# Kernel optimization log

Hardware: AMD Instinct MI355X
Metric: run time of the kernel (lower is better)

Reference implementation:

```python
import jax, jax.numpy as jnp
import numpy as np

EPS = 1e-6

def _complex_log(x):
    # real = log(clamp_min(|x|, eps)); imag = pi where x < 0 else 0
    real = jnp.log(jnp.maximum(jnp.abs(x), EPS))
    imag = jnp.where(x < 0, np.float32(np.pi), np.float32(0.0))
    return jax.lax.complex(real, imag)

def _clogaddexp(a, b):
    # stable log(exp(a)+exp(b)) for complex a, b (shift by max of real parts)
    m = jnp.maximum(a.real, b.real)
    return jnp.log(jnp.exp(a - m) + jnp.exp(b - m)) + m

def _min_gru(h, g):
    # log-space minGRU linear recurrence over the last axis
    log_coeffs = -jax.nn.softplus(g)                      # [..., L] real
    log_values = _complex_log(h) - jax.nn.softplus(-g)    # [..., L] complex
    a_star = jnp.cumsum(log_coeffs, axis=-1)              # [..., L] real
    z = log_values - a_star                               # complex
    log_h0_plus_b_star = jax.lax.associative_scan(_clogaddexp, z, axis=-1)
    log_h = a_star + log_h0_plus_b_star
    return jnp.exp(log_h).real

def _min_gru_bidirectional(x):
    # x: [B, H, L] with H divisible by 4
    H = x.shape[1]
    fore, back = x[:, : H // 2], x[:, H // 2 :]
    fh, fg = fore[:, : H // 4], fore[:, H // 4 :]
    back = jnp.flip(back, axis=2)  # matches torch .flip(2) for [B,H,L]
    bh, bg = back[:, : H // 4], back[:, H // 4 :]
    out_f = _min_gru(fh, fg)
    out_b = jnp.flip(_min_gru(bh, bg), axis=2)
    return jnp.concatenate([out_f, out_b], axis=1)  # [B, H/2, L]

def setup_inputs() -> dict:
    key = jax.random.key(0)
    x = jax.random.normal(key, (16, 512, 4096), dtype=jnp.float32)
    return {"x": x}

def reference(x):
    return _min_gru_bidirectional(x)
```

## Files before the change

kernel.cpp:

```cpp
#include <hip/hip_runtime.h>


#define T_LEN 4096
#define CHUNK 16
#define NTHR 256

__global__ __launch_bounds__(NTHR) void mingru_bidir_kernel(
    const float* __restrict__ x, float* __restrict__ out) {
  const int row = blockIdx.x;
  const int b   = row >> 8;
  const int c   = row & 255;
  const int tid = threadIdx.x;
  const int lane = tid & 63;
  const int wid  = tid >> 6;
  const bool bwd = (c >= 128);
  const int j = c & 127;

  const float* __restrict__ hptr =
      x + ((size_t)b * 512 + (bwd ? 256 : 0) + j) * T_LEN;
  const float* __restrict__ gptr =
      x + ((size_t)b * 512 + (bwd ? 384 : 128) + j) * T_LEN;
  float* __restrict__ optr = out + ((size_t)b * 256 + c) * T_LEN;

  const int t0 = bwd ? (T_LEN - CHUNK - (tid << 4)) : (tid << 4);

  float cc[CHUNK], vv[CHUNK];

  #pragma unroll
  for (int q = 0; q < 4; ++q) {
    const float4 h4 = *reinterpret_cast<const float4*>(hptr + t0 + 4 * q);
    const float4 g4 = *reinterpret_cast<const float4*>(gptr + t0 + 4 * q);
    const float hs[4] = {h4.x, h4.y, h4.z, h4.w};
    const float gs[4] = {g4.x, g4.y, g4.z, g4.w};
    #pragma unroll
    for (int r = 0; r < 4; ++r) {
      const int e = 4 * q + r;
      const float h = hs[r];
      const float g = gs[r];
      const float ah = fmaxf(fabsf(h), 1e-6f);
      const float hp = (h < 0.0f) ? -ah : ah;
      const float eg  = __expf(-fabsf(g));
      const float inv = __builtin_amdgcn_rcpf(1.0f + eg);
      const float sg  = (g >= 0.0f) ? inv : eg * inv;
      cc[e] = 1.0f - sg;
      vv[e] = sg * hp;
    }
  }

  if (bwd) {
    #pragma unroll
    for (int e = 0; e < CHUNK / 2; ++e) {
      float t1 = cc[e]; cc[e] = cc[CHUNK - 1 - e]; cc[CHUNK - 1 - e] = t1;
      float t2 = vv[e]; vv[e] = vv[CHUNK - 1 - e]; vv[CHUNK - 1 - e] = t2;
    }
  }

  float C = cc[0], V = vv[0];
  #pragma unroll
  for (int e = 1; e < CHUNK; ++e) {
    V = cc[e] * V + vv[e];
    C = C * cc[e];
  }

  #pragma unroll
  for (int off = 1; off < 64; off <<= 1) {
    const float pc = __shfl_up(C, off);
    const float pv = __shfl_up(V, off);
    if (lane >= off) {
      V = C * pv + V;
      C = C * pc;
    }
  }

  __shared__ float sC[4], sV[4];
  if (lane == 63) { sC[wid] = C; sV[wid] = V; }
  __syncthreads();
  float acc = 0.0f;
  for (int w = 0; w < wid; ++w) acc = sC[w] * acc + sV[w];

  const float pC = __shfl_up(C, 1);
  const float pV = __shfl_up(V, 1);
  const float incoming = (lane == 0) ? acc : pC * acc + pV;

  float st = incoming;
  #pragma unroll
  for (int e = 0; e < CHUNK; ++e) {
    st = cc[e] * st + vv[e];
    vv[e] = st;
  }

  if (bwd) {
    #pragma unroll
    for (int e = 0; e < CHUNK / 2; ++e) {
      float t2 = vv[e]; vv[e] = vv[CHUNK - 1 - e]; vv[CHUNK - 1 - e] = t2;
    }
  }

  #pragma unroll
  for (int q = 0; q < 4; ++q) {
    *reinterpret_cast<float4*>(optr + t0 + 4 * q) =
        make_float4(vv[4 * q], vv[4 * q + 1], vv[4 * q + 2], vv[4 * q + 3]);
  }
}

extern "C" void kernel_launch(void* const* d_in, const int* in_sizes, int n_in,
                              void* d_out, int out_size, void* d_ws, size_t ws_size,
                              hipStream_t stream) {
  const float* x = (const float*)d_in[0];
  float* out = (float*)d_out;
  const int rows = 16 * 256;
  mingru_bidir_kernel<<<rows, NTHR, 0, stream>>>(x, out);
}
```

Baseline: 39.27 us.

## Interleave per-thread chunks for coalesced loads and run four independent scans

Each thread now loads four float4 pieces spaced 1024 elements apart instead of 16 contiguous elements, so a wavefront reads contiguous memory on each access. The row is therefore split into four independent 1024-long segments, each scanned across the block with its own wave shuffle scan and cross-wave combine, and the segments are chained serially. Backward rows use shfl_down scans instead of reversed register order. Launch bounds now request higher occupancy. The cost is four times as many shuffle-scan steps and more shared-memory combine work.

```diff
diff --git a/kernel.cpp b/kernel.cpp
--- a/kernel.cpp
+++ b/kernel.cpp
@@ -2,10 +2,9 @@
 
 
 #define T_LEN 4096
-#define CHUNK 16
 #define NTHR 256
 
-__global__ __launch_bounds__(NTHR) void mingru_bidir_kernel(
+__global__ __launch_bounds__(NTHR, 6) void mingru_bidir_kernel(
     const float* __restrict__ x, float* __restrict__ out) {
   const int row = blockIdx.x;
   const int b   = row >> 8;
@@ -22,19 +21,17 @@
       x + ((size_t)b * 512 + (bwd ? 384 : 128) + j) * T_LEN;
   float* __restrict__ optr = out + ((size_t)b * 256 + c) * T_LEN;
 
-  const int t0 = bwd ? (T_LEN - CHUNK - (tid << 4)) : (tid << 4);
-
-  float cc[CHUNK], vv[CHUNK];
+  float cc[4][4], vv[4][4];
 
   #pragma unroll
   for (int q = 0; q < 4; ++q) {
-    const float4 h4 = *reinterpret_cast<const float4*>(hptr + t0 + 4 * q);
-    const float4 g4 = *reinterpret_cast<const float4*>(gptr + t0 + 4 * q);
+    const int m0 = (q << 10) + (tid << 2);
+    const float4 h4 = *reinterpret_cast<const float4*>(hptr + m0);
+    const float4 g4 = *reinterpret_cast<const float4*>(gptr + m0);
     const float hs[4] = {h4.x, h4.y, h4.z, h4.w};
     const float gs[4] = {g4.x, g4.y, g4.z, g4.w};
     #pragma unroll
     for (int r = 0; r < 4; ++r) {
-      const int e = 4 * q + r;
       const float h = hs[r];
       const float g = gs[r];
       const float ah = fmaxf(fabsf(h), 1e-6f);
@@ -42,64 +39,103 @@
       const float eg  = __expf(-fabsf(g));
       const float inv = __builtin_amdgcn_rcpf(1.0f + eg);
       const float sg  = (g >= 0.0f) ? inv : eg * inv;
-      cc[e] = 1.0f - sg;
-      vv[e] = sg * hp;
+      const float co  = 1.0f - sg;
+      const float va  = sg * hp;
+      if (bwd) { cc[q][3 - r] = co; vv[q][3 - r] = va; }
+      else     { cc[q][r]     = co; vv[q][r]     = va; }
     }
   }
 
   if (bwd) {
     #pragma unroll
-    for (int e = 0; e < CHUNK / 2; ++e) {
-      float t1 = cc[e]; cc[e] = cc[CHUNK - 1 - e]; cc[CHUNK - 1 - e] = t1;
-      float t2 = vv[e]; vv[e] = vv[CHUNK - 1 - e]; vv[CHUNK - 1 - e] = t2;
+    for (int e = 0; e < 4; ++e) {
+      float t;
+      t = cc[0][e]; cc[0][e] = cc[3][e]; cc[3][e] = t;
+      t = cc[1][e]; cc[1][e] = cc[2][e]; cc[2][e] = t;
+      t = vv[0][e]; vv[0][e] = vv[3][e]; vv[3][e] = t;
+      t = vv[1][e]; vv[1][e] = vv[2][e]; vv[2][e] = t;
     }
   }
 
-  float C = cc[0], V = vv[0];
+  float C[4], V[4];
   #pragma unroll
-  for (int e = 1; e < CHUNK; ++e) {
-    V = cc[e] * V + vv[e];
-    C = C * cc[e];
-  }
-
-  #pragma unroll
-  for (int off = 1; off < 64; off <<= 1) {
-    const float pc = __shfl_up(C, off);
-    const float pv = __shfl_up(V, off);
-    if (lane >= off) {
-      V = C * pv + V;
-      C = C * pc;
+  for (int q = 0; q < 4; ++q) {
+    C[q] = cc[q][0]; V[q] = vv[q][0];
+    #pragma unroll
+    for (int e = 1; e < 4; ++e) {
+      V[q] = cc[q][e] * V[q] + vv[q][e];
+      C[q] = C[q] * cc[q][e];
     }
   }
 
-  __shared__ float sC[4], sV[4];
-  if (lane == 63) { sC[wid] = C; sV[wid] = V; }
-  __syncthreads();
-  float acc = 0.0f;
-  for (int w = 0; w < wid; ++w) acc = sC[w] * acc + sV[w];
-
-  const float pC = __shfl_up(C, 1);
-  const float pV = __shfl_up(V, 1);
-  const float incoming = (lane == 0) ? acc : pC * acc + pV;
-
-  float st = incoming;
-  #pragma unroll
-  for (int e = 0; e < CHUNK; ++e) {
-    st = cc[e] * st + vv[e];
-    vv[e] = st;
+  if (!bwd) {
+    #pragma unroll
+    for (int q = 0; q < 4; ++q) {
+      #pragma unroll
+      for (int off = 1; off < 64; off <<= 1) {
+        const float pc = __shfl_up(C[q], off);
+        const float pv = __shfl_up(V[q], off);
+        if (lane >= off) { V[q] = C[q] * pv + V[q]; C[q] = C[q] * pc; }
+      }
+    }
+  } else {
+    #pragma unroll
+    for (int q = 0; q < 4; ++q) {
+      #pragma unroll
+      for (int off = 1; off < 64; off <<= 1) {
+        const float pc = __shfl_down(C[q], off);
+        const float pv = __shfl_down(V[q], off);
+        if (lane < 64 - off) { V[q] = C[q] * pv + V[q]; C[q] = C[q] * pc; }
+      }
+    }
   }
 
-  if (bwd) {
+  __shared__ float sC[4][4], sV[4][4];
+  if (lane == (bwd ? 0 : 63)) {
     #pragma unroll
-    for (int e = 0; e < CHUNK / 2; ++e) {
-      float t2 = vv[e]; vv[e] = vv[CHUNK - 1 - e]; vv[CHUNK - 1 - e] = t2;
+    for (int q = 0; q < 4; ++q) { sC[wid][q] = C[q]; sV[wid][q] = V[q]; }
+  }
+  __syncthreads();
+
+  float myin[4];
+  float s = 0.0f;
+  if (!bwd) {
+    #pragma unroll
+    for (int q = 0; q < 4; ++q) {
+      #pragma unroll
+      for (int w = 0; w < 4; ++w) {
+        if (w == wid) myin[q] = s;
+        s = sC[w][q] * s + sV[w][q];
+      }
+    }
+  } else {
+    #pragma unroll
+    for (int q = 0; q < 4; ++q) {
+      #pragma unroll
+      for (int w = 3; w >= 0; --w) {
+        if (w == wid) myin[q] = s;
+        s = sC[w][q] * s + sV[w][q];
+      }
     }
   }
 
   #pragma unroll
   for (int q = 0; q < 4; ++q) {
-    *reinterpret_cast<float4*>(optr + t0 + 4 * q) =
-        make_float4(vv[4 * q], vv[4 * q + 1], vv[4 * q + 2], vv[4 * q + 3]);
+    const float pc = bwd ? __shfl_down(C[q], 1) : __shfl_up(C[q], 1);
+    const float pv = bwd ? __shfl_down(V[q], 1) : __shfl_up(V[q], 1);
+    const bool first = bwd ? (lane == 63) : (lane == 0);
+    float st = first ? myin[q] : pc * myin[q] + pv;
+
+    float o[4];
+    #pragma unroll
+    for (int e = 0; e < 4; ++e) {
+      st = cc[q][e] * st + vv[q][e];
+      o[e] = st;
+    }
+    const int qmem = bwd ? 3 - q : q;
+    const float4 o4 = bwd ? make_float4(o[3], o[2], o[1], o[0])
+                          : make_float4(o[0], o[1], o[2], o[3]);
+    *reinterpret_cast<float4*>(optr + (qmem << 10) + (tid << 2)) = o4;
   }
 }
 
```

After: 36.47 us. 1.08x faster.

## Use 1024 threads per row with 4 elements each and direction-aware scan

Applied to the files above, without the earlier changes.

Each row is now processed by 1024 threads, each owning a single float4 instead of 16 elements. The backward direction runs its wave and cross-wave scans in reverse order (shfl_down, descending wave loop) instead of flipping register arrays. The aim is coalesced contiguous loads per wave and more memory parallelism. The cost is a 16-wave block with a longer serial cross-wave combine and more scan work relative to the loads.

```diff
diff --git a/kernel.cpp b/kernel.cpp
--- a/kernel.cpp
+++ b/kernel.cpp
@@ -2,8 +2,7 @@
 
 
 #define T_LEN 4096
-#define CHUNK 16
-#define NTHR 256
+#define NTHR 1024
 
 __global__ __launch_bounds__(NTHR) void mingru_bidir_kernel(
     const float* __restrict__ x, float* __restrict__ out) {
@@ -22,85 +21,86 @@
       x + ((size_t)b * 512 + (bwd ? 384 : 128) + j) * T_LEN;
   float* __restrict__ optr = out + ((size_t)b * 256 + c) * T_LEN;
 
-  const int t0 = bwd ? (T_LEN - CHUNK - (tid << 4)) : (tid << 4);
+  const int m0 = tid << 2;
 
-  float cc[CHUNK], vv[CHUNK];
+  const float4 h4 = *reinterpret_cast<const float4*>(hptr + m0);
+  const float4 g4 = *reinterpret_cast<const float4*>(gptr + m0);
+  const float hs[4] = {h4.x, h4.y, h4.z, h4.w};
+  const float gs[4] = {g4.x, g4.y, g4.z, g4.w};
 
+  float cc[4], vv[4];
   #pragma unroll
-  for (int q = 0; q < 4; ++q) {
-    const float4 h4 = *reinterpret_cast<const float4*>(hptr + t0 + 4 * q);
-    const float4 g4 = *reinterpret_cast<const float4*>(gptr + t0 + 4 * q);
-    const float hs[4] = {h4.x, h4.y, h4.z, h4.w};
-    const float gs[4] = {g4.x, g4.y, g4.z, g4.w};
-    #pragma unroll
-    for (int r = 0; r < 4; ++r) {
-      const int e = 4 * q + r;
-      const float h = hs[r];
-      const float g = gs[r];
-      const float ah = fmaxf(fabsf(h), 1e-6f);
-      const float hp = (h < 0.0f) ? -ah : ah;
-      const float eg  = __expf(-fabsf(g));
-      const float inv = __builtin_amdgcn_rcpf(1.0f + eg);
-      const float sg  = (g >= 0.0f) ? inv : eg * inv;
-      cc[e] = 1.0f - sg;
-      vv[e] = sg * hp;
-    }
-  }
-
-  if (bwd) {
-    #pragma unroll
-    for (int e = 0; e < CHUNK / 2; ++e) {
-      float t1 = cc[e]; cc[e] = cc[CHUNK - 1 - e]; cc[CHUNK - 1 - e] = t1;
-      float t2 = vv[e]; vv[e] = vv[CHUNK - 1 - e]; vv[CHUNK - 1 - e] = t2;
-    }
+  for (int r = 0; r < 4; ++r) {
+    const float h = hs[r];
+    const float g = gs[r];
+    const float ah = fmaxf(fabsf(h), 1e-6f);
+    const float hp = (h < 0.0f) ? -ah : ah;
+    const float eg  = __expf(-fabsf(g));
+    const float inv = __builtin_amdgcn_rcpf(1.0f + eg);
+    const float sg  = (g >= 0.0f) ? inv : eg * inv;
+    const float co  = 1.0f - sg;
+    const float va  = sg * hp;
+    if (bwd) { cc[3 - r] = co; vv[3 - r] = va; }
+    else     { cc[r]     = co; vv[r]     = va; }
   }
 
   float C = cc[0], V = vv[0];
   #pragma unroll
-  for (int e = 1; e < CHUNK; ++e) {
+  for (int e = 1; e < 4; ++e) {
     V = cc[e] * V + vv[e];
     C = C * cc[e];
   }
 
-  #pragma unroll
-  for (int off = 1; off < 64; off <<= 1) {
-    const float pc = __shfl_up(C, off);
-    const float pv = __shfl_up(V, off);
-    if (lane >= off) {
-      V = C * pv + V;
-      C = C * pc;
+  if (!bwd) {
+    #pragma unroll
+    for (int off = 1; off < 64; off <<= 1) {
+      const float pc = __shfl_up(C, off);
+      const float pv = __shfl_up(V, off);
+      if (lane >= off) { V = C * pv + V; C = C * pc; }
+    }
+  } else {
+    #pragma unroll
+    for (int off = 1; off < 64; off <<= 1) {
+      const float pc = __shfl_down(C, off);
+      const float pv = __shfl_down(V, off);
+      if (lane < 64 - off) { V = C * pv + V; C = C * pc; }
     }
   }
 
-  __shared__ float sC[4], sV[4];
-  if (lane == 63) { sC[wid] = C; sV[wid] = V; }
+  __shared__ float sC[16], sV[16];
+  if (lane == (bwd ? 0 : 63)) { sC[wid] = C; sV[wid] = V; }
   __syncthreads();
-  float acc = 0.0f;
-  for (int w = 0; w < wid; ++w) acc = sC[w] * acc + sV[w];
 
-  const float pC = __shfl_up(C, 1);
-  const float pV = __shfl_up(V, 1);
-  const float incoming = (lane == 0) ? acc : pC * acc + pV;
-
-  float st = incoming;
-  #pragma unroll
-  for (int e = 0; e < CHUNK; ++e) {
-    st = cc[e] * st + vv[e];
-    vv[e] = st;
-  }
-
-  if (bwd) {
+  float myin = 0.0f;
+  float s = 0.0f;
+  if (!bwd) {
     #pragma unroll
-    for (int e = 0; e < CHUNK / 2; ++e) {
-      float t2 = vv[e]; vv[e] = vv[CHUNK - 1 - e]; vv[CHUNK - 1 - e] = t2;
+    for (int w = 0; w < 16; ++w) {
+      if (w == wid) myin = s;
+      s = sC[w] * s + sV[w];
+    }
+  } else {
+    #pragma unroll
+    for (int w = 15; w >= 0; --w) {
+      if (w == wid) myin = s;
+      s = sC[w] * s + sV[w];
     }
   }
 
+  const float pc = bwd ? __shfl_down(C, 1) : __shfl_up(C, 1);
+  const float pv = bwd ? __shfl_down(V, 1) : __shfl_up(V, 1);
+  const bool first = bwd ? (lane == 63) : (lane == 0);
+  float st = first ? myin : pc * myin + pv;
+
+  float o[4];
   #pragma unroll
-  for (int q = 0; q < 4; ++q) {
-    *reinterpret_cast<float4*>(optr + t0 + 4 * q) =
-        make_float4(vv[4 * q], vv[4 * q + 1], vv[4 * q + 2], vv[4 * q + 3]);
+  for (int e = 0; e < 4; ++e) {
+    st = cc[e] * st + vv[e];
+    o[e] = st;
   }
+  const float4 o4 = bwd ? make_float4(o[3], o[2], o[1], o[0])
+                        : make_float4(o[0], o[1], o[2], o[3]);
+  *reinterpret_cast<float4*>(optr + m0) = o4;
 }
 
 extern "C" void kernel_launch(void* const* d_in, const int* in_sizes, int n_in,
```

After: 35.00 us. -10.9%, faster.
